# Kernel optimization log

Hardware: AMD Instinct MI355X
Metric: run time of the kernel (lower is better)

Reference implementation:

```python
import jax, jax.numpy as jnp
import numpy as np

B, H, W = 16, 384, 1280
HW = H * W
K = 131072  # number of top-k selected pixels per batch element


def setup_inputs() -> dict:
    key = jax.random.key(0)
    k1, k2, k3 = jax.random.split(key, 3)
    # depth map in a plausible metric range
    depth = jax.random.uniform(k1, (B, 1, H, W), jnp.float32, 0.1, 80.0)
    inv_K = jax.random.normal(k2, (B, 4, 4), jnp.float32)
    top_k_indices = jax.random.randint(k3, (B, K), 0, HW)
    # non-trainable buffer: homogeneous pixel coordinates [B, 3, HW]
    gx, gy = np.meshgrid(np.arange(W), np.arange(H), indexing='xy')
    pix = np.stack([gx.reshape(-1), gy.reshape(-1), np.ones(HW)], axis=0).astype(np.float32)  # [3, HW]
    pix_coords = jnp.tile(jnp.asarray(pix)[None], (B, 1, 1))  # [B, 3, HW]
    return {"depth": depth, "inv_K": inv_K, "pix_coords": pix_coords,
            "top_k_indices": top_k_indices}


def reference(depth, inv_K, pix_coords, top_k_indices):
    b, k = top_k_indices.shape
    idx1 = top_k_indices[:, None, :]                      # [B, 1, K]
    idx3 = jnp.broadcast_to(idx1, (b, 3, k))              # [B, 3, K]
    # gather selected homogeneous pixel coords -> [B, 3, K]
    pix_sel = jnp.take_along_axis(pix_coords, idx3, axis=2)
    # small batched 3x3 matmul: rays in camera frame
    cam_points = jnp.einsum('bij,bjk->bik', inv_K[:, :3, :3], pix_sel)  # [B, 3, K]
    # gather selected depths -> [B, 1, K]
    depth_flat = depth.reshape(b, 1, -1)
    depth_sel = jnp.take_along_axis(depth_flat, idx1, axis=2)
    cam_points = depth_sel * cam_points
    ones_sel = jnp.ones_like(depth_sel)                   # ones buffer gather is all ones
    return jnp.concatenate([cam_points, ones_sel], axis=1)  # [B, 4, K]
```

## Files before the change

kernel.cpp:

```cpp
#include <hip/hip_runtime.h>


#define BB 16
#define HH 384
#define WW 1280
#define HWSZ (HH * WW)
#define KK 131072
#define NXCD 8
#define BLOCKS_PER_BATCH (KK / (256 * 4))
#define TOTAL_BLOCKS (BB * BLOCKS_PER_BATCH)

typedef float v4f __attribute__((ext_vector_type(4)));
typedef int   v4i __attribute__((ext_vector_type(4)));

__global__ __launch_bounds__(256) void backproject_kernel(
    const float* __restrict__ depth,
    const float* __restrict__ invK,
    const int*   __restrict__ topk,
    float*       __restrict__ out)
{
    const int xcd  = blockIdx.x & (NXCD - 1);
    const int slot = blockIdx.x >> 3;
    const int logical = xcd * (TOTAL_BLOCKS / NXCD) + slot;
    const int b   = logical >> 7;
    const int blk = logical & 127;
    const int k0  = blk * 1024 + threadIdx.x * 4;

    const float* __restrict__ M = invK + b * 16;
    const float m00 = M[0], m01 = M[1], m02 = M[2];
    const float m10 = M[4], m11 = M[5], m12 = M[6];
    const float m20 = M[8], m21 = M[9], m22 = M[10];

    const v4i idx4 = __builtin_nontemporal_load(
        reinterpret_cast<const v4i*>(topk + b * KK + k0));
    const float* __restrict__ db = depth + b * HWSZ;

    float ox[4], oy[4], oz[4];
#pragma unroll
    for (int j = 0; j < 4; ++j) {
        const int idx = idx4[j];
        const float d  = db[idx];
        const float gx = (float)(idx % WW);
        const float gy = (float)(idx / WW);
        const float c0 = fmaf(m00, gx, fmaf(m01, gy, m02));
        const float c1 = fmaf(m10, gx, fmaf(m11, gy, m12));
        const float c2 = fmaf(m20, gx, fmaf(m21, gy, m22));
        ox[j] = d * c0;
        oy[j] = d * c1;
        oz[j] = d * c2;
    }

    float* __restrict__ ob = out + (size_t)b * 4 * KK + k0;
    v4f vx = {ox[0], ox[1], ox[2], ox[3]};
    v4f vy = {oy[0], oy[1], oy[2], oy[3]};
    v4f vz = {oz[0], oz[1], oz[2], oz[3]};
    v4f vw = {1.f, 1.f, 1.f, 1.f};
    __builtin_nontemporal_store(vx, reinterpret_cast<v4f*>(ob + 0 * KK));
    __builtin_nontemporal_store(vy, reinterpret_cast<v4f*>(ob + 1 * KK));
    __builtin_nontemporal_store(vz, reinterpret_cast<v4f*>(ob + 2 * KK));
    __builtin_nontemporal_store(vw, reinterpret_cast<v4f*>(ob + 3 * KK));
}

extern "C" void kernel_launch(void* const* d_in, const int* in_sizes, int n_in,
                              void* d_out, int out_size, void* d_ws, size_t ws_size,
                              hipStream_t stream) {
    const float* depth = (const float*)d_in[0];
    const float* invK  = (const float*)d_in[1];
    const int*   topk  = (const int*)d_in[3];
    float* out = (float*)d_out;

    backproject_kernel<<<TOTAL_BLOCKS, 256, 0, stream>>>(depth, invK, topk, out);
}
```

Before: 18.30 us.

## Add pre-pass kernel streaming depth into L2 and writing ones row

Adds a warm kernel that reads the full depth map with coalesced vector loads so it sits in cache, and writes the constant ones row of the output. The gather kernel then hits the warmed cache for its random depth reads and no longer stores the fourth row. The cost is a second launch and a full sequential read of depth, about 31 MB, more than the random gathers would touch. It also groups the four depth loads ahead of the arithmetic.

After: 22.58 us. 23.4% more time.

```diff
diff --git a/kernel.cpp b/kernel.cpp
--- a/kernel.cpp
+++ b/kernel.cpp
@@ -5,13 +5,47 @@
 #define HH 384
 #define WW 1280
 #define HWSZ (HH * WW)
+#define HW4 (HWSZ / 4)
 #define KK 131072
 #define NXCD 8
 #define BLOCKS_PER_BATCH (KK / (256 * 4))
 #define TOTAL_BLOCKS (BB * BLOCKS_PER_BATCH)
+#define WARM_F4_PER_BLOCK (HW4 / BLOCKS_PER_BATCH)
 
 typedef float v4f __attribute__((ext_vector_type(4)));
 typedef int   v4i __attribute__((ext_vector_type(4)));
+
+__device__ __forceinline__ void xcd_map(int bid, int& b, int& blk) {
+    const int xcd  = bid & (NXCD - 1);
+    const int slot = bid >> 3;
+    const int logical = xcd * (TOTAL_BLOCKS / NXCD) + slot;
+    b   = logical >> 7;
+    blk = logical & 127;
+}
+
+__global__ __launch_bounds__(256) void warm_kernel(
+    const float* __restrict__ depth, float* __restrict__ out)
+{
+    int b, blk;
+    xcd_map(blockIdx.x, b, blk);
+
+    const v4f* __restrict__ d4 = reinterpret_cast<const v4f*>(depth) + b * HW4;
+    float acc = 0.f;
+#pragma unroll
+    for (int it = 0; it < 4; ++it) {
+        const int i = blk * WARM_F4_PER_BLOCK + it * 256 + threadIdx.x;
+        if (it < 3 || i < (blk + 1) * WARM_F4_PER_BLOCK) {
+            const v4f v = d4[i];
+            acc += v[0] + v[1] + v[2] + v[3];
+        }
+    }
+    asm volatile("" :: "v"(acc));
+
+    const int k0 = blk * 1024 + threadIdx.x * 4;
+    float* __restrict__ ob = out + (size_t)b * 4 * KK + 3 * KK + k0;
+    v4f vw = {1.f, 1.f, 1.f, 1.f};
+    __builtin_nontemporal_store(vw, reinterpret_cast<v4f*>(ob));
+}
 
 __global__ __launch_bounds__(256) void backproject_kernel(
     const float* __restrict__ depth,
@@ -19,12 +53,9 @@
     const int*   __restrict__ topk,
     float*       __restrict__ out)
 {
-    const int xcd  = blockIdx.x & (NXCD - 1);
-    const int slot = blockIdx.x >> 3;
-    const int logical = xcd * (TOTAL_BLOCKS / NXCD) + slot;
-    const int b   = logical >> 7;
-    const int blk = logical & 127;
-    const int k0  = blk * 1024 + threadIdx.x * 4;
+    int b, blk;
+    xcd_map(blockIdx.x, b, blk);
+    const int k0 = blk * 1024 + threadIdx.x * 4;
 
     const float* __restrict__ M = invK + b * 16;
     const float m00 = M[0], m01 = M[1], m02 = M[2];
@@ -35,30 +66,29 @@
         reinterpret_cast<const v4i*>(topk + b * KK + k0));
     const float* __restrict__ db = depth + b * HWSZ;
 
+    const int idxs[4] = {idx4[0], idx4[1], idx4[2], idx4[3]};
+    float d[4];
+#pragma unroll
+    for (int j = 0; j < 4; ++j) d[j] = db[idxs[j]];
+
     float ox[4], oy[4], oz[4];
 #pragma unroll
     for (int j = 0; j < 4; ++j) {
-        const int idx = idx4[j];
-        const float d  = db[idx];
+        const int idx = idxs[j];
         const float gx = (float)(idx % WW);
         const float gy = (float)(idx / WW);
-        const float c0 = fmaf(m00, gx, fmaf(m01, gy, m02));
-        const float c1 = fmaf(m10, gx, fmaf(m11, gy, m12));
-        const float c2 = fmaf(m20, gx, fmaf(m21, gy, m22));
-        ox[j] = d * c0;
-        oy[j] = d * c1;
-        oz[j] = d * c2;
+        ox[j] = d[j] * fmaf(m00, gx, fmaf(m01, gy, m02));
+        oy[j] = d[j] * fmaf(m10, gx, fmaf(m11, gy, m12));
+        oz[j] = d[j] * fmaf(m20, gx, fmaf(m21, gy, m22));
     }
 
     float* __restrict__ ob = out + (size_t)b * 4 * KK + k0;
     v4f vx = {ox[0], ox[1], ox[2], ox[3]};
     v4f vy = {oy[0], oy[1], oy[2], oy[3]};
     v4f vz = {oz[0], oz[1], oz[2], oz[3]};
-    v4f vw = {1.f, 1.f, 1.f, 1.f};
     __builtin_nontemporal_store(vx, reinterpret_cast<v4f*>(ob + 0 * KK));
     __builtin_nontemporal_store(vy, reinterpret_cast<v4f*>(ob + 1 * KK));
     __builtin_nontemporal_store(vz, reinterpret_cast<v4f*>(ob + 2 * KK));
-    __builtin_nontemporal_store(vw, reinterpret_cast<v4f*>(ob + 3 * KK));
 }
 
 extern "C" void kernel_launch(void* const* d_in, const int* in_sizes, int n_in,
@@ -69,5 +99,6 @@
     const int*   topk  = (const int*)d_in[3];
     float* out = (float*)d_out;
 
+    warm_kernel<<<TOTAL_BLOCKS, 256, 0, stream>>>(depth, out);
     backproject_kernel<<<TOTAL_BLOCKS, 256, 0, stream>>>(depth, invK, topk, out);
 }
```
